# Optimization experiments

Hardware: AMD Instinct MI355X
Metric: run time of the kernel (lower is better)

The kernel has to match this reference:

```python
import jax, jax.numpy as jnp
import numpy as np

N_NODES = 200_000
N_EDGES = 400_000
EXTRA_NNZ = 3 * N_EDGES
IN_CH = 14
HID = 128
ALPHA = -1.5  # HNHN edge-cardinality exponent
BETA = -0.5   # HNHN node-cardinality exponent


def setup_inputs() -> dict:
    key = jax.random.key(0)
    ks = jax.random.split(key, 16)
    # COO incidence: guarantee every node and every edge has >= 1 entry so
    # cardinality^negative_power stays finite (like real molecular hypergraphs).
    base_rows = jnp.arange(N_NODES, dtype=jnp.int32)
    base_cols = jnp.arange(N_NODES, dtype=jnp.int32) % N_EDGES
    edge_rows = jax.random.randint(ks[0], (N_EDGES,), 0, N_NODES, dtype=jnp.int32)
    edge_cols = jnp.arange(N_EDGES, dtype=jnp.int32)
    rnd_rows = jax.random.randint(ks[1], (EXTRA_NNZ,), 0, N_NODES, dtype=jnp.int32)
    rnd_cols = jax.random.randint(ks[2], (EXTRA_NNZ,), 0, N_EDGES, dtype=jnp.int32)
    inc_rows = jnp.concatenate([base_rows, edge_rows, rnd_rows])
    inc_cols = jnp.concatenate([base_cols, edge_cols, rnd_cols])
    inc_vals = jnp.ones(inc_rows.shape[0], dtype=jnp.float32)

    def glorot(k, shape):
        fan_in, fan_out = shape[0], shape[-1]
        s = jnp.sqrt(2.0 / (fan_in + fan_out)).astype(jnp.float32)
        return jax.random.normal(k, shape, dtype=jnp.float32) * s

    return {
        "x_0": jax.random.normal(ks[3], (N_NODES, IN_CH), dtype=jnp.float32),
        "inc_rows": inc_rows,
        "inc_cols": inc_cols,
        "inc_vals": inc_vals,
        "w0_l1": glorot(ks[4], (IN_CH, HID)),
        "w1_l1": glorot(ks[5], (HID, HID)),
        "b1_l1": glorot(ks[6], (1, HID)),
        "b0_l1": glorot(ks[7], (1, HID)),
        "w0_l2": glorot(ks[8], (HID, HID)),
        "w1_l2": glorot(ks[9], (HID, HID)),
        "b1_l2": glorot(ks[10], (1, HID)),
        "b0_l2": glorot(ks[11], (1, HID)),
        "lin_w": glorot(ks[12], (HID, 1)),
        "lin_b": jnp.zeros((1,), dtype=jnp.float32),
    }


def _normalized_values(inc_rows, inc_cols, inc_vals):
    """HNHN alpha/beta normalization of B (node<-edge) and B^T (edge<-node)."""
    seg = jax.ops.segment_sum
    deg_e = seg(inc_vals, inc_cols, num_segments=N_EDGES)   # |e| per hyperedge
    deg_v = seg(inc_vals, inc_rows, num_segments=N_NODES)   # |v| per node
    e_card = deg_e ** ALPHA
    n_card = deg_v ** BETA
    denom_v = seg(inc_vals * e_card[inc_cols], inc_rows, num_segments=N_NODES)  # (B @ e_card)
    denom_e = seg(inc_vals * n_card[inc_rows], inc_cols, num_segments=N_EDGES)  # (B^T @ n_card)
    # D0_left_alpha^{-1} B D1_right_alpha   and   D1_left_beta^{-1} B^T D0_right_beta
    vals_v_from_e = inc_vals * e_card[inc_cols] / denom_v[inc_rows]
    vals_e_from_v = inc_vals * n_card[inc_rows] / denom_e[inc_cols]
    return vals_v_from_e, vals_e_from_v


def reference(x_0, inc_rows, inc_cols, inc_vals,
              w0_l1, w1_l1, b1_l1, b0_l1,
              w0_l2, w1_l2, b1_l2, b0_l2,
              lin_w, lin_b):
    seg = jax.ops.segment_sum
    vals_v_from_e, vals_e_from_v = _normalized_values(inc_rows, inc_cols, inc_vals)

    def layer(x0, w0, w1, b1, b0):
        # node -> hyperedge: x1 = sigma(Bt_norm @ (x0 W0) + b1)
        m = x0 @ w0                                        # [N_NODES, HID]
        x1 = jax.nn.sigmoid(
            seg(vals_e_from_v[:, None] * m[inc_rows], inc_cols, num_segments=N_EDGES) + b1
        )                                                  # [N_EDGES, HID]
        # hyperedge -> node: x0' = sigma(B_norm @ (x1 W1) + b0)
        m2 = x1 @ w1
        x0n = jax.nn.sigmoid(
            seg(vals_v_from_e[:, None] * m2[inc_cols], inc_rows, num_segments=N_NODES) + b0
        )                                                  # [N_NODES, HID]
        return x0n, x1

    x0, x1 = layer(x_0, w0_l1, w1_l1, b1_l1, b0_l1)
    x0, x1 = layer(x0, w0_l2, w1_l2, b1_l2, b0_l2)
    pooled = jnp.max(x0, axis=0)                           # graph-level max pool [HID]
    return pooled @ lin_w + lin_b                          # [1]
```

## Files before the change

### kernel.cpp

```cpp
#include <hip/hip_runtime.h>
#include <hip/hip_bf16.h>

#define N_NODES 200000
#define N_EDGES 400000
#define HID 128

#define SHIFT 10
#define NB_E 391
#define NB_V 196
#define NBT (NB_E + NB_V)
#define CAP_E 6144
#define CAP_V 10240

typedef unsigned int u32;
typedef unsigned short u16;
typedef unsigned char u8;
typedef long long i64;
typedef __attribute__((ext_vector_type(4))) float f32x4;
typedef __attribute__((ext_vector_type(2))) float f32x2;

__device__ inline float sigmoidf(float v) { return 1.0f / (1.0f + __expf(-v)); }

__device__ inline u32 pk4_fp8(float f0, float f1, float f2, float f3) {
  u32 v = __builtin_amdgcn_cvt_pk_fp8_f32(f0, f1, 0, false);
  v = __builtin_amdgcn_cvt_pk_fp8_f32(f2, f3, v, true);
  return v;
}

__device__ inline void acc16_fp8(const uint4& q, float wv, f32x2* a) {
#pragma unroll
  for (int h = 0; h < 4; ++h) {
    u32 u = (&q.x)[h];
    a[h * 2 + 0] += __builtin_amdgcn_cvt_pk_f32_fp8(u, false) * wv;
    a[h * 2 + 1] += __builtin_amdgcn_cvt_pk_f32_fp8(u, true) * wv;
  }
}

__global__ __launch_bounds__(256) void bin_mm14_kernel(
    const int* __restrict__ rows, const int* __restrict__ cols,
    const float* __restrict__ vals, u32* __restrict__ bkE,
    u32* __restrict__ bkV, int2* __restrict__ tmp_e, int2* __restrict__ tmp_v,
    int nnz, int nbBin, const float* __restrict__ x0,
    const float* __restrict__ w14, u8* __restrict__ U, int N) {
  __shared__ u32 smem[14 * HID];
  const int tid = threadIdx.x;

  if ((int)blockIdx.x >= nbBin) {
    float* ws = (float*)smem;
    for (int i = tid; i < 14 * HID; i += 256) ws[i] = w14[i];
    __syncthreads();
    const int row = ((int)blockIdx.x - nbBin) * 8 + (tid >> 5);
    const int c4 = (tid & 31) << 2;
    if (row >= N) return;
    const float* xr = x0 + (size_t)row * 14;
    float a0 = 0.f, a1 = 0.f, a2 = 0.f, a3 = 0.f;
#pragma unroll
    for (int k = 0; k < 14; ++k) {
      const float xv = xr[k];
      const float* wr = ws + k * HID + c4;
      a0 = fmaf(xv, wr[0], a0);
      a1 = fmaf(xv, wr[1], a1);
      a2 = fmaf(xv, wr[2], a2);
      a3 = fmaf(xv, wr[3], a3);
    }
    *(u32*)(U + (size_t)row * HID + c4) = pk4_fp8(a0, a1, a2, a3);
    return;
  }

  u32* h = smem;
  u32* base = smem + NBT;
  for (int j = tid; j < NBT; j += 256) h[j] = 0;
  __syncthreads();
  const int i0 = blockIdx.x * 4096;
  for (int k = 0; k < 16; ++k) {
    int i = i0 + k * 256 + tid;
    if (i < nnz) {
      atomicAdd(&h[cols[i] >> SHIFT], 1u);
      atomicAdd(&h[NB_E + (rows[i] >> SHIFT)], 1u);
    }
  }
  __syncthreads();
  for (int j = tid; j < NBT; j += 256) {
    u32 n = h[j];
    base[j] = n ? ((j < NB_E) ? atomicAdd(&bkE[j], n)
                              : atomicAdd(&bkV[j - NB_E], n))
                : 0;
    h[j] = 0;
  }
  __syncthreads();
  for (int k = 0; k < 16; ++k) {
    int i = i0 + k * 256 + tid;
    if (i < nnz) {
      int c = cols[i], r = rows[i];
      int vb = __float_as_int(vals[i]);
      int be = c >> SHIFT;
      int bv = NB_E + (r >> SHIFT);
      u32 le = atomicAdd(&h[be], 1u);
      tmp_e[(size_t)be * CAP_E + base[be] + le] =
          make_int2(((c & 1023) << 19) | r, vb);
      u32 lv = atomicAdd(&h[bv], 1u);
      tmp_v[(size_t)(bv - NB_E) * CAP_V + base[bv] + lv] =
          make_int2(((r & 1023) << 19) | c, vb);
    }
  }
}

__global__ __launch_bounds__(512) void scan_all_kernel(
    u32* __restrict__ bkE, u32* __restrict__ bkV, u32* __restrict__ ptr_e,
    u32* __restrict__ ptr_v, u32 nnz) {
  if (blockIdx.x == 2) {
    if (threadIdx.x == 0) {
      bkE[NB_E] = nnz;
      bkV[NB_V] = nnz;
      ptr_e[N_EDGES] = nnz;
      ptr_v[N_NODES] = nnz;
    }
    return;
  }
  u32* blk = (blockIdx.x == 0) ? bkE : bkV;
  const int n = (blockIdx.x == 0) ? NB_E : NB_V;
  __shared__ u32 tmp[512];
  int t = threadIdx.x;
  u32 v = (t < n) ? blk[t] : 0;
  tmp[t] = v;
  __syncthreads();
  for (int d = 1; d < 512; d <<= 1) {
    u32 x = (t >= d) ? tmp[t - d] : 0;
    __syncthreads();
    tmp[t] += x;
    __syncthreads();
  }
  if (t < n) blk[t] = tmp[t] - v;
}

template <bool EDGE>
__global__ __launch_bounds__(512) void build_kernel(
    const int2* __restrict__ tmp, int cap, const u32* __restrict__ bukBase,
    u32* __restrict__ ptr, int2* __restrict__ ent, float* __restrict__ card,
    const float* __restrict__ ncard, int S) {
  __shared__ u32 loc[1024];
  __shared__ u32 sstart[1024];
  __shared__ u32 aux[512];
  const int tid = threadIdx.x;
  const int c0 = blockIdx.x << SHIFT;
  const int nseg = min(1024, S - c0);
  const u32 eb = bukBase[blockIdx.x], ee = bukBase[blockIdx.x + 1];
  const u32 cnt = ee - eb;
  const int2* tp = tmp + (size_t)blockIdx.x * cap;
  loc[tid] = 0;
  loc[tid + 512] = 0;
  __syncthreads();
  for (u32 j = tid; j < cnt; j += 512)
    atomicAdd(&loc[(u32)tp[j].x >> 19], 1u);
  __syncthreads();
  u32 a0 = loc[2 * tid], a1 = loc[2 * tid + 1];
  u32 T = a0 + a1;
  aux[tid] = T;
  __syncthreads();
  for (int d = 1; d < 512; d <<= 1) {
    u32 x = (tid >= d) ? aux[tid - d] : 0;
    __syncthreads();
    aux[tid] += x;
    __syncthreads();
  }
  u32 off = aux[tid] - T;
  loc[2 * tid] = off;
  loc[2 * tid + 1] = off + a0;
  sstart[2 * tid] = off;
  sstart[2 * tid + 1] = off + a0;
  __syncthreads();
  for (int k = tid; k < nseg; k += 512) ptr[c0 + k] = eb + loc[k];
  __syncthreads();
  for (u32 j = tid; j < cnt; j += 512) {
    int2 e = tp[j];
    u32 s = (u32)e.x >> 19;
    u32 p = atomicAdd(&loc[s], 1u);
    ent[eb + p] = make_int2(e.x & 0x7FFFF, e.y);
  }
  __syncthreads();
  for (int k = tid; k < nseg; k += 512) {
    u32 s0 = eb + sstart[k], s1 = eb + loc[k];
    float s = 0.f;
    for (u32 j = s0; j < s1; ++j) s += __int_as_float(ent[j].y);
    float t = rsqrtf(s);
    card[c0 + k] = EDGE ? t * t * t : t;
    if (EDGE) {
      float d = 0.f;
      for (u32 j = s0; j < s1; ++j) {
        int2 en = ent[j];
        d += __int_as_float(en.y) * ncard[en.x];
      }
      float inv = 1.f / d;
      for (u32 j = s0; j < s1; ++j) {
        int2 en = ent[j];
        ent[j].y = __float_as_int(__int_as_float(en.y) * ncard[en.x] * inv);
      }
    }
  }
}

__global__ __launch_bounds__(256) void segV_kernel(
    const u32* __restrict__ ptr_v, int2* __restrict__ ent_v,
    const float* __restrict__ e_card) {
  int t = blockIdx.x * 256 + threadIdx.x;
  int i = t >> 1;
  int half = t & 1;
  if (i >= N_NODES) return;
  u32 b = ptr_v[i], e = ptr_v[i + 1];
  float s = 0.f;
  for (u32 j = b + half; j < e; j += 2) {
    int2 en = ent_v[j];
    s += __int_as_float(en.y) * e_card[en.x];
  }
  s += __shfl_xor(s, 1);
  float inv = 1.f / s;
  for (u32 j = b + half; j < e; j += 2) {
    int2 en = ent_v[j];
    ent_v[j].y = __float_as_int(__int_as_float(en.y) * e_card[en.x] * inv);
  }
}


__device__ inline void load_wfrags(const float* __restrict__ w, int lo, int hi,
                                   i64 wf[8][4]) {
#pragma unroll
  for (int n = 0; n < 8; ++n)
#pragma unroll
    for (int t = 0; t < 4; ++t) {
      const float* wp = w + (size_t)(t * 32 + hi * 8) * HID + n * 16 + lo;
      u32 w0 = pk4_fp8(wp[0], wp[HID], wp[2 * HID], wp[3 * HID]);
      u32 w1 = pk4_fp8(wp[4 * HID], wp[5 * HID], wp[6 * HID], wp[7 * HID]);
      wf[n][t] = (i64)w0 | ((i64)w1 << 32);
    }
}

template <bool SIG, bool POOL>
__global__ __launch_bounds__(256, 1) void im128_mfma_kernel(
    u8* __restrict__ buf, const float* __restrict__ w,
    const float* __restrict__ b, u32* __restrict__ pooled, int R) {
  const int tid = threadIdx.x;
  const int wave = tid >> 6;
  const int lo = tid & 15;
  const int hi = (tid & 63) >> 4;
  i64 wf[8][4];
  load_wfrags(w, lo, hi, wf);
  float bias[8];
  if (SIG) {
#pragma unroll
    for (int n = 0; n < 8; ++n) bias[n] = b[n * 16 + lo];
  }
  float pm[8];
#pragma unroll
  for (int n = 0; n < 8; ++n) pm[n] = 0.f;

  for (int rb = blockIdx.x * 64 + wave * 16; rb < R; rb += gridDim.x * 64) {
    const u8* xp = buf + (size_t)(rb + lo) * HID + hi * 8;
    i64 a0 = *(const i64*)(xp);
    i64 a1 = *(const i64*)(xp + 32);
    i64 a2 = *(const i64*)(xp + 64);
    i64 a3 = *(const i64*)(xp + 96);
    u8* yp = buf + (size_t)(rb + hi * 4) * HID + lo;
#pragma unroll
    for (int n = 0; n < 8; ++n) {
      f32x4 c = {0.f, 0.f, 0.f, 0.f};
      c = __builtin_amdgcn_mfma_f32_16x16x32_fp8_fp8(a0, wf[n][0], c, 0, 0, 0);
      c = __builtin_amdgcn_mfma_f32_16x16x32_fp8_fp8(a1, wf[n][1], c, 0, 0, 0);
      c = __builtin_amdgcn_mfma_f32_16x16x32_fp8_fp8(a2, wf[n][2], c, 0, 0, 0);
      c = __builtin_amdgcn_mfma_f32_16x16x32_fp8_fp8(a3, wf[n][3], c, 0, 0, 0);
#pragma unroll
      for (int r = 0; r < 4; ++r) {
        float v = SIG ? sigmoidf(c[r] + bias[n]) : c[r];
        if (POOL) {
          pm[n] = fmaxf(pm[n], v);
        } else {
          u32 q = __builtin_amdgcn_cvt_pk_fp8_f32(v, v, 0, false);
          yp[(size_t)r * HID + n * 16] = (u8)q;
        }
      }
    }
  }

  if (POOL) {
    __shared__ u32 pmax[HID];
    for (int i = tid; i < HID; i += 256) pmax[i] = 0;
    __syncthreads();
#pragma unroll
    for (int n = 0; n < 8; ++n)
      atomicMax(&pmax[n * 16 + lo], __float_as_uint(pm[n]));
    __syncthreads();
    if (tid < HID) atomicMax(&pooled[tid], pmax[tid]);
  }
}


template <bool SIG>
__global__ __launch_bounds__(256) void gather128_kernel(
    const u32* __restrict__ ptr, const int2* __restrict__ ent,
    const u8* __restrict__ src, const float* __restrict__ b,
    u8* __restrict__ dst, int S) {
  long long t = (long long)blockIdx.x * 256 + threadIdx.x;
  int r = (int)(t >> 3);
  if (r >= S) return;
  const int c16 = (int)(t & 7) << 4;
  u32 beg = ptr[r], end = ptr[r + 1];
  f32x2 a[8];
#pragma unroll
  for (int i = 0; i < 8; ++i) a[i] = (f32x2){0.f, 0.f};
  u32 j = beg;
  for (; j + 2 <= end; j += 2) {
    int2 e0 = ent[j];
    int2 e1 = ent[j + 1];
    const uint4 q0 = *(const uint4*)(src + (size_t)e0.x * HID + c16);
    const uint4 q1 = *(const uint4*)(src + (size_t)e1.x * HID + c16);
    acc16_fp8(q0, __int_as_float(e0.y), a);
    acc16_fp8(q1, __int_as_float(e1.y), a);
  }
  if (j < end) {
    int2 e0 = ent[j];
    const uint4 q0 = *(const uint4*)(src + (size_t)e0.x * HID + c16);
    acc16_fp8(q0, __int_as_float(e0.y), a);
  }
  float o[16];
#pragma unroll
  for (int h = 0; h < 4; ++h) {
    o[h * 4 + 0] = a[h * 2 + 0].x;
    o[h * 4 + 1] = a[h * 2 + 0].y;
    o[h * 4 + 2] = a[h * 2 + 1].x;
    o[h * 4 + 3] = a[h * 2 + 1].y;
  }
  if (SIG) {
#pragma unroll
    for (int h = 0; h < 4; ++h) {
      float4 bb = *(const float4*)(b + c16 + h * 4);
      o[h * 4 + 0] = sigmoidf(o[h * 4 + 0] + bb.x);
      o[h * 4 + 1] = sigmoidf(o[h * 4 + 1] + bb.y);
      o[h * 4 + 2] = sigmoidf(o[h * 4 + 2] + bb.z);
      o[h * 4 + 3] = sigmoidf(o[h * 4 + 3] + bb.w);
    }
  }
  uint4 pk;
  pk.x = pk4_fp8(o[0], o[1], o[2], o[3]);
  pk.y = pk4_fp8(o[4], o[5], o[6], o[7]);
  pk.z = pk4_fp8(o[8], o[9], o[10], o[11]);
  pk.w = pk4_fp8(o[12], o[13], o[14], o[15]);
  *(uint4*)(dst + (size_t)r * HID + c16) = pk;
}


__global__ __launch_bounds__(128) void final_kernel(
    const u32* __restrict__ pooled, const float* __restrict__ lin_w,
    const float* __restrict__ lin_b, float* __restrict__ out) {
  __shared__ float red[64];
  int t = threadIdx.x;
  float v = __uint_as_float(pooled[t]) * lin_w[t];
  if (t >= 64) red[t - 64] = v;
  __syncthreads();
  if (t < 64) {
    v += red[t];
#pragma unroll
    for (int off = 32; off > 0; off >>= 1) v += __shfl_down(v, off);
    if (t == 0) out[0] = v + lin_b[0];
  }
}

__global__ void diag_kernel(float* out, float v) { out[0] = v; }


extern "C" void kernel_launch(void* const* d_in, const int* in_sizes, int n_in,
                              void* d_out, int out_size, void* d_ws, size_t ws_size,
                              hipStream_t stream) {
  const float* x0     = (const float*)d_in[0];
  const int*   rows   = (const int*)d_in[1];
  const int*   cols   = (const int*)d_in[2];
  const float* vals   = (const float*)d_in[3];
  const float* w0_l1  = (const float*)d_in[4];
  const float* w1_l1  = (const float*)d_in[5];
  const float* b1_l1  = (const float*)d_in[6];
  const float* b0_l1  = (const float*)d_in[7];
  const float* w0_l2  = (const float*)d_in[8];
  const float* w1_l2  = (const float*)d_in[9];
  const float* b1_l2  = (const float*)d_in[10];
  const float* b0_l2  = (const float*)d_in[11];
  const float* lin_w  = (const float*)d_in[12];
  const float* lin_b  = (const float*)d_in[13];
  float* out = (float*)d_out;
  const int nnz = in_sizes[1];

  char* wsp = (char*)d_ws;
  size_t off = 0;
  auto carve = [&](size_t bytes) -> char* {
    char* p = wsp + off;
    off = (off + bytes + 511) & ~(size_t)511;
    return p;
  };
  float* n_card  = (float*)carve((size_t)N_NODES * 4);
  float* e_card  = (float*)carve((size_t)N_EDGES * 4);
  u32*   ptr_v   = (u32*)carve((size_t)(N_NODES + 1) * 4);
  u32*   ptr_e   = (u32*)carve((size_t)(N_EDGES + 1) * 4);
  u32*   bkE     = (u32*)carve((NB_E + 1) * 4);
  u32*   bkV     = (u32*)carve((NB_V + 1) * 4);
  int2*  ent_v   = (int2*)carve((size_t)nnz * 8);
  int2*  ent_e   = (int2*)carve((size_t)nnz * 8);
  u32*   pooled  = (u32*)carve(HID * 4);
  u8*    bufN    = (u8*)carve((size_t)N_NODES * HID);
  u8*    bufE    = (u8*)carve((size_t)N_EDGES * HID);
  int2*  tmp_e   = (int2*)carve((size_t)NB_E * CAP_E * 8);
  int2*  tmp_v   = (int2*)carve((size_t)NB_V * CAP_V * 8);

  if (off > ws_size) {
    diag_kernel<<<1, 1, 0, stream>>>(out, (float)(ws_size >> 20));
    return;
  }

  hipMemsetAsync(bkE, 0, (NB_E + 1) * 4, stream);
  hipMemsetAsync(bkV, 0, (NB_V + 1) * 4, stream);
  hipMemsetAsync(pooled, 0, HID * 4, stream);

  const int nbBin = (nnz + 4095) / 4096;
  const int nbMM14 = (N_NODES + 7) / 8;

  bin_mm14_kernel<<<nbBin + nbMM14, 256, 0, stream>>>(
      rows, cols, vals, bkE, bkV, tmp_e, tmp_v, nnz, nbBin,
      x0, w0_l1, bufN, N_NODES);
  scan_all_kernel<<<3, 512, 0, stream>>>(bkE, bkV, ptr_e, ptr_v, (u32)nnz);
  build_kernel<false><<<NB_V, 512, 0, stream>>>(tmp_v, CAP_V, bkV, ptr_v,
                                                ent_v, n_card, nullptr, N_NODES);
  build_kernel<true><<<NB_E, 512, 0, stream>>>(tmp_e, CAP_E, bkE, ptr_e,
                                               ent_e, e_card, n_card, N_EDGES);
  segV_kernel<<<(2 * N_NODES + 255) / 256, 256, 0, stream>>>(ptr_v, ent_v, e_card);

  const int nbE8 = (int)(((long long)N_EDGES * 8 + 255) / 256);
  const int nbN8 = (int)(((long long)N_NODES * 8 + 255) / 256);

  gather128_kernel<true><<<nbE8, 256, 0, stream>>>(ptr_e, ent_e, bufN,
                                                   b1_l1, bufE, N_EDGES);
  gather128_kernel<false><<<nbN8, 256, 0, stream>>>(ptr_v, ent_v, bufE,
                                                    nullptr, bufN, N_NODES);
  im128_mfma_kernel<true, false><<<1024, 256, 0, stream>>>(bufN, w1_l1, b0_l1,
                                                           nullptr, N_NODES);

  im128_mfma_kernel<false, false><<<1024, 256, 0, stream>>>(bufN, w0_l2, nullptr,
                                                            nullptr, N_NODES);
  gather128_kernel<true><<<nbE8, 256, 0, stream>>>(ptr_e, ent_e, bufN,
                                                   b1_l2, bufE, N_EDGES);
  gather128_kernel<false><<<nbN8, 256, 0, stream>>>(ptr_v, ent_v, bufE,
                                                    nullptr, bufN, N_NODES);
  im128_mfma_kernel<true, true><<<1024, 256, 0, stream>>>(bufN, w1_l2, b0_l2,
                                                          pooled, N_NODES);

  final_kernel<<<1, 128, 0, stream>>>(pooled, lin_w, lin_b, out);
}
```

Measured before the change: 453.4 us.

## Split binning into per-direction blocks with LDS-staged coalesced scatter

Measured after the change: 498.2 us. 9.9% more time.

```diff
diff --git a/kernel.cpp b/kernel.cpp
--- a/kernel.cpp
+++ b/kernel.cpp
@@ -8,9 +8,9 @@
 #define SHIFT 10
 #define NB_E 391
 #define NB_V 196
-#define NBT (NB_E + NB_V)
 #define CAP_E 6144
 #define CAP_V 10240
+#define BINSZ 4096
 
 typedef unsigned int u32;
 typedef unsigned short u16;
@@ -40,16 +40,22 @@
     const int* __restrict__ rows, const int* __restrict__ cols,
     const float* __restrict__ vals, u32* __restrict__ bkE,
     u32* __restrict__ bkV, int2* __restrict__ tmp_e, int2* __restrict__ tmp_v,
-    int nnz, int nbBin, const float* __restrict__ x0,
+    int nnz, int nbBinE, int nbBinV, const float* __restrict__ x0,
     const float* __restrict__ w14, u8* __restrict__ U, int N) {
-  __shared__ u32 smem[14 * HID];
+  __shared__ int2 stage[BINSZ];
+  __shared__ u32 dsti[BINSZ];
+  __shared__ u32 h[NB_E];
+  __shared__ u32 pe[NB_E + 1];
+  __shared__ u32 gb[NB_E];
+  __shared__ u32 aux[256];
   const int tid = threadIdx.x;
-
-  if ((int)blockIdx.x >= nbBin) {
-    float* ws = (float*)smem;
+  const int bid = blockIdx.x;
+
+  if (bid >= nbBinE + nbBinV) {
+    float* ws = (float*)stage;
     for (int i = tid; i < 14 * HID; i += 256) ws[i] = w14[i];
     __syncthreads();
-    const int row = ((int)blockIdx.x - nbBin) * 8 + (tid >> 5);
+    const int row = (bid - nbBinE - nbBinV) * 8 + (tid >> 5);
     const int c4 = (tid & 31) << 2;
     if (row >= N) return;
     const float* xr = x0 + (size_t)row * 14;
@@ -67,48 +73,67 @@
     return;
   }
 
-  u32* h = smem;
-  u32* base = smem + NBT;
-  for (int j = tid; j < NBT; j += 256) h[j] = 0;
-  __syncthreads();
-  const int i0 = blockIdx.x * 4096;
-  for (int k = 0; k < 16; ++k) {
+  const bool ES = bid < nbBinE;
+  const int blk = ES ? bid : bid - nbBinE;
+  const int NB = ES ? NB_E : NB_V;
+  const int CAP = ES ? CAP_E : CAP_V;
+  const int* __restrict__ key = ES ? cols : rows;
+  const int* __restrict__ oth = ES ? rows : cols;
+  u32* __restrict__ bk = ES ? bkE : bkV;
+  int2* __restrict__ tmp = ES ? tmp_e : tmp_v;
+
+  for (int j = tid; j < NB; j += 256) h[j] = 0;
+  __syncthreads();
+  const int i0 = blk * BINSZ;
+  const int total = min(BINSZ, nnz - i0);
+#pragma unroll
+  for (int k = 0; k < BINSZ / 256; ++k) {
+    int i = i0 + k * 256 + tid;
+    if (i < nnz) atomicAdd(&h[key[i] >> SHIFT], 1u);
+  }
+  __syncthreads();
+  u32 a0 = (2 * tid < NB) ? h[2 * tid] : 0;
+  u32 a1 = (2 * tid + 1 < NB) ? h[2 * tid + 1] : 0;
+  u32 T = a0 + a1;
+  aux[tid] = T;
+  __syncthreads();
+  for (int d = 1; d < 256; d <<= 1) {
+    u32 x = (tid >= d) ? aux[tid - d] : 0;
+    __syncthreads();
+    aux[tid] += x;
+    __syncthreads();
+  }
+  u32 off = aux[tid] - T;
+  if (2 * tid < NB) pe[2 * tid] = off;
+  if (2 * tid + 1 < NB) pe[2 * tid + 1] = off + a0;
+  for (int j = tid; j < NB; j += 256) {
+    u32 n = h[j];
+    gb[j] = n ? atomicAdd(&bk[j], n) : 0;
+    h[j] = 0;
+  }
+  __syncthreads();
+#pragma unroll
+  for (int k = 0; k < BINSZ / 256; ++k) {
     int i = i0 + k * 256 + tid;
     if (i < nnz) {
-      atomicAdd(&h[cols[i] >> SHIFT], 1u);
-      atomicAdd(&h[NB_E + (rows[i] >> SHIFT)], 1u);
-    }
-  }
-  __syncthreads();
-  for (int j = tid; j < NBT; j += 256) {
-    u32 n = h[j];
-    base[j] = n ? ((j < NB_E) ? atomicAdd(&bkE[j], n)
-                              : atomicAdd(&bkV[j - NB_E], n))
-                : 0;
-    h[j] = 0;
-  }
-  __syncthreads();
-  for (int k = 0; k < 16; ++k) {
-    int i = i0 + k * 256 + tid;
-    if (i < nnz) {
-      int c = cols[i], r = rows[i];
-      int vb = __float_as_int(vals[i]);
-      int be = c >> SHIFT;
-      int bv = NB_E + (r >> SHIFT);
-      u32 le = atomicAdd(&h[be], 1u);
-      tmp_e[(size_t)be * CAP_E + base[be] + le] =
-          make_int2(((c & 1023) << 19) | r, vb);
-      u32 lv = atomicAdd(&h[bv], 1u);
-      tmp_v[(size_t)(bv - NB_E) * CAP_V + base[bv] + lv] =
-          make_int2(((r & 1023) << 19) | c, vb);
-    }
-  }
+      int kk = key[i];
+      int b = kk >> SHIFT;
+      u32 lr = atomicAdd(&h[b], 1u);
+      u32 pos = pe[b] + lr;
+      stage[pos] = make_int2(((kk & 1023) << 19) | oth[i],
+                             __float_as_int(vals[i]));
+      dsti[pos] = (u32)b * CAP + gb[b] + lr;
+    }
+  }
+  __syncthreads();
+  for (int t = tid; t < total; t += 256) tmp[dsti[t]] = stage[t];
 }
 
 __global__ __launch_bounds__(512) void scan_all_kernel(
     u32* __restrict__ bkE, u32* __restrict__ bkV, u32* __restrict__ ptr_e,
-    u32* __restrict__ ptr_v, u32 nnz) {
+    u32* __restrict__ ptr_v, u32* __restrict__ pooled, u32 nnz) {
   if (blockIdx.x == 2) {
+    if (threadIdx.x < HID) pooled[threadIdx.x] = 0;
     if (threadIdx.x == 0) {
       bkE[NB_E] = nnz;
       bkV[NB_V] = nnz;
@@ -412,17 +437,15 @@
     return;
   }
 
-  hipMemsetAsync(bkE, 0, (NB_E + 1) * 4, stream);
-  hipMemsetAsync(bkV, 0, (NB_V + 1) * 4, stream);
-  hipMemsetAsync(pooled, 0, HID * 4, stream);
-
-  const int nbBin = (nnz + 4095) / 4096;
+  hipMemsetAsync(bkE, 0, (size_t)((char*)ent_v - (char*)bkE), stream);
+
+  const int nbBin = (nnz + BINSZ - 1) / BINSZ;
   const int nbMM14 = (N_NODES + 7) / 8;
 
-  bin_mm14_kernel<<<nbBin + nbMM14, 256, 0, stream>>>(
-      rows, cols, vals, bkE, bkV, tmp_e, tmp_v, nnz, nbBin,
+  bin_mm14_kernel<<<2 * nbBin + nbMM14, 256, 0, stream>>>(
+      rows, cols, vals, bkE, bkV, tmp_e, tmp_v, nnz, nbBin, nbBin,
       x0, w0_l1, bufN, N_NODES);
-  scan_all_kernel<<<3, 512, 0, stream>>>(bkE, bkV, ptr_e, ptr_v, (u32)nnz);
+  scan_all_kernel<<<3, 512, 0, stream>>>(bkE, bkV, ptr_e, ptr_v, pooled, (u32)nnz);
   build_kernel<false><<<NB_V, 512, 0, stream>>>(tmp_v, CAP_V, bkV, ptr_v,
                                                 ent_v, n_card, nullptr, N_NODES);
   build_kernel<true><<<NB_E, 512, 0, stream>>>(tmp_e, CAP_E, bkE, ptr_e,
```

## Reorder gather rows by segment length to balance wavefront work

Applied to the files above, without the earlier changes.

New measurement: 478.3 us. 1.05x slower.

```diff
diff --git a/kernel.cpp b/kernel.cpp
--- a/kernel.cpp
+++ b/kernel.cpp
@@ -11,6 +11,7 @@
 #define NBT (NB_E + NB_V)
 #define CAP_E 6144
 #define CAP_V 10240
+#define BINSZ 4096
 
 typedef unsigned int u32;
 typedef unsigned short u16;
@@ -71,8 +72,8 @@
   u32* base = smem + NBT;
   for (int j = tid; j < NBT; j += 256) h[j] = 0;
   __syncthreads();
-  const int i0 = blockIdx.x * 4096;
-  for (int k = 0; k < 16; ++k) {
+  const int i0 = blockIdx.x * BINSZ;
+  for (int k = 0; k < BINSZ / 256; ++k) {
     int i = i0 + k * 256 + tid;
     if (i < nnz) {
       atomicAdd(&h[cols[i] >> SHIFT], 1u);
@@ -88,7 +89,7 @@
     h[j] = 0;
   }
   __syncthreads();
-  for (int k = 0; k < 16; ++k) {
+  for (int k = 0; k < BINSZ / 256; ++k) {
     int i = i0 + k * 256 + tid;
     if (i < nnz) {
       int c = cols[i], r = rows[i];
@@ -107,8 +108,9 @@
 
 __global__ __launch_bounds__(512) void scan_all_kernel(
     u32* __restrict__ bkE, u32* __restrict__ bkV, u32* __restrict__ ptr_e,
-    u32* __restrict__ ptr_v, u32 nnz) {
+    u32* __restrict__ ptr_v, u32* __restrict__ pooled, u32 nnz) {
   if (blockIdx.x == 2) {
+    if (threadIdx.x < HID) pooled[threadIdx.x] = 0;
     if (threadIdx.x == 0) {
       bkE[NB_E] = nnz;
       bkV[NB_V] = nnz;
@@ -137,10 +139,11 @@
 __global__ __launch_bounds__(512) void build_kernel(
     const int2* __restrict__ tmp, int cap, const u32* __restrict__ bukBase,
     u32* __restrict__ ptr, int2* __restrict__ ent, float* __restrict__ card,
-    const float* __restrict__ ncard, int S) {
+    const float* __restrict__ ncard, u32* __restrict__ lcnt, int S) {
   __shared__ u32 loc[1024];
   __shared__ u32 sstart[1024];
   __shared__ u32 aux[512];
+  __shared__ u32 lh[16];
   const int tid = threadIdx.x;
   const int c0 = blockIdx.x << SHIFT;
   const int nseg = min(1024, S - c0);
@@ -149,6 +152,7 @@
   const int2* tp = tmp + (size_t)blockIdx.x * cap;
   loc[tid] = 0;
   loc[tid + 512] = 0;
+  if (tid < 16) lh[tid] = 0;
   __syncthreads();
   for (u32 j = tid; j < cnt; j += 512)
     atomicAdd(&loc[(u32)tp[j].x >> 19], 1u);
@@ -179,6 +183,8 @@
   }
   __syncthreads();
   for (int k = tid; k < nseg; k += 512) {
+    u32 len = loc[k] - sstart[k];
+    atomicAdd(&lh[min(len - 1, 15u)], 1u);
     u32 s0 = eb + sstart[k], s1 = eb + loc[k];
     float s = 0.f;
     for (u32 j = s0; j < s1; ++j) s += __int_as_float(ent[j].y);
@@ -197,6 +203,48 @@
       }
     }
   }
+  __syncthreads();
+  if (tid < 16 && lh[tid]) atomicAdd(&lcnt[tid], lh[tid]);
+}
+
+__global__ void scan32_kernel(u32* __restrict__ lcntE, u32* __restrict__ lcntV) {
+  u32* a = (threadIdx.x == 0) ? lcntE : lcntV;
+  u32 s = 0;
+  for (int i = 0; i < 16; ++i) {
+    u32 v = a[i];
+    a[i] = s;
+    s += v;
+  }
+}
+
+__global__ __launch_bounds__(256) void perm_place_kernel(
+    const u32* __restrict__ ptr_e, const u32* __restrict__ ptr_v,
+    u32* __restrict__ curE, u32* __restrict__ curV,
+    u32* __restrict__ permE, u32* __restrict__ permV, int nbE) {
+  const int bid = blockIdx.x;
+  const bool ES = bid < nbE;
+  const u32* ptr = ES ? ptr_e : ptr_v;
+  u32* cur = ES ? curE : curV;
+  u32* perm = ES ? permE : permV;
+  const int S = ES ? N_EDGES : N_NODES;
+  const int i = (ES ? bid : bid - nbE) * 256 + threadIdx.x;
+  __shared__ u32 lh[16];
+  __shared__ u32 base[16];
+  if (threadIdx.x < 16) lh[threadIdx.x] = 0;
+  __syncthreads();
+  int b = 0;
+  u32 lr = 0;
+  if (i < S) {
+    u32 len = ptr[i + 1] - ptr[i];
+    b = (int)min(len - 1, 15u);
+    lr = atomicAdd(&lh[b], 1u);
+  }
+  __syncthreads();
+  if (threadIdx.x < 16)
+    base[threadIdx.x] =
+        lh[threadIdx.x] ? atomicAdd(&cur[threadIdx.x], lh[threadIdx.x]) : 0;
+  __syncthreads();
+  if (i < S) perm[base[b] + lr] = (u32)i;
 }
 
 __global__ __launch_bounds__(256) void segV_kernel(
@@ -296,11 +344,12 @@
 template <bool SIG>
 __global__ __launch_bounds__(256) void gather128_kernel(
     const u32* __restrict__ ptr, const int2* __restrict__ ent,
-    const u8* __restrict__ src, const float* __restrict__ b,
-    u8* __restrict__ dst, int S) {
+    const u32* __restrict__ perm, const u8* __restrict__ src,
+    const float* __restrict__ b, u8* __restrict__ dst, int S) {
   long long t = (long long)blockIdx.x * 256 + threadIdx.x;
-  int r = (int)(t >> 3);
-  if (r >= S) return;
+  int rid = (int)(t >> 3);
+  if (rid >= S) return;
+  const int r = (int)perm[rid];
   const int c16 = (int)(t & 7) << 4;
   u32 beg = ptr[r], end = ptr[r + 1];
   f32x2 a[8];
@@ -399,8 +448,12 @@
   u32*   ptr_e   = (u32*)carve((size_t)(N_EDGES + 1) * 4);
   u32*   bkE     = (u32*)carve((NB_E + 1) * 4);
   u32*   bkV     = (u32*)carve((NB_V + 1) * 4);
+  u32*   lcntE   = (u32*)carve(16 * 4);
+  u32*   lcntV   = (u32*)carve(16 * 4);
   int2*  ent_v   = (int2*)carve((size_t)nnz * 8);
   int2*  ent_e   = (int2*)carve((size_t)nnz * 8);
+  u32*   permE   = (u32*)carve((size_t)N_EDGES * 4);
+  u32*   permV   = (u32*)carve((size_t)N_NODES * 4);
   u32*   pooled  = (u32*)carve(HID * 4);
   u8*    bufN    = (u8*)carve((size_t)N_NODES * HID);
   u8*    bufE    = (u8*)carve((size_t)N_EDGES * HID);
@@ -412,38 +465,41 @@
     return;
   }
 
-  hipMemsetAsync(bkE, 0, (NB_E + 1) * 4, stream);
-  hipMemsetAsync(bkV, 0, (NB_V + 1) * 4, stream);
-  hipMemsetAsync(pooled, 0, HID * 4, stream);
-
-  const int nbBin = (nnz + 4095) / 4096;
+  hipMemsetAsync(bkE, 0, (size_t)((char*)ent_v - (char*)bkE), stream);
+
+  const int nbBin = (nnz + BINSZ - 1) / BINSZ;
   const int nbMM14 = (N_NODES + 7) / 8;
+  const int nbPermE = (N_EDGES + 255) / 256;
+  const int nbPermV = (N_NODES + 255) / 256;
 
   bin_mm14_kernel<<<nbBin + nbMM14, 256, 0, stream>>>(
       rows, cols, vals, bkE, bkV, tmp_e, tmp_v, nnz, nbBin,
       x0, w0_l1, bufN, N_NODES);
-  scan_all_kernel<<<3, 512, 0, stream>>>(bkE, bkV, ptr_e, ptr_v, (u32)nnz);
-  build_kernel<false><<<NB_V, 512, 0, stream>>>(tmp_v, CAP_V, bkV, ptr_v,
-                                                ent_v, n_card, nullptr, N_NODES);
-  build_kernel<true><<<NB_E, 512, 0, stream>>>(tmp_e, CAP_E, bkE, ptr_e,
-                                               ent_e, e_card, n_card, N_EDGES);
+  scan_all_kernel<<<3, 512, 0, stream>>>(bkE, bkV, ptr_e, ptr_v, pooled, (u32)nnz);
+  build_kernel<false><<<NB_V, 512, 0, stream>>>(tmp_v, CAP_V, bkV, ptr_v, ent_v,
+                                                n_card, nullptr, lcntV, N_NODES);
+  build_kernel<true><<<NB_E, 512, 0, stream>>>(tmp_e, CAP_E, bkE, ptr_e, ent_e,
+                                               e_card, n_card, lcntE, N_EDGES);
+  scan32_kernel<<<1, 2, 0, stream>>>(lcntE, lcntV);
+  perm_place_kernel<<<nbPermE + nbPermV, 256, 0, stream>>>(
+      ptr_e, ptr_v, lcntE, lcntV, permE, permV, nbPermE);
   segV_kernel<<<(2 * N_NODES + 255) / 256, 256, 0, stream>>>(ptr_v, ent_v, e_card);
 
   const int nbE8 = (int)(((long long)N_EDGES * 8 + 255) / 256);
   const int nbN8 = (int)(((long long)N_NODES * 8 + 255) / 256);
 
-  gather128_kernel<true><<<nbE8, 256, 0, stream>>>(ptr_e, ent_e, bufN,
+  gather128_kernel<true><<<nbE8, 256, 0, stream>>>(ptr_e, ent_e, permE, bufN,
                                                    b1_l1, bufE, N_EDGES);
-  gather128_kernel<false><<<nbN8, 256, 0, stream>>>(ptr_v, ent_v, bufE,
+  gather128_kernel<false><<<nbN8, 256, 0, stream>>>(ptr_v, ent_v, permV, bufE,
                                                     nullptr, bufN, N_NODES);
   im128_mfma_kernel<true, false><<<1024, 256, 0, stream>>>(bufN, w1_l1, b0_l1,
                                                            nullptr, N_NODES);
 
   im128_mfma_kernel<false, false><<<1024, 256, 0, stream>>>(bufN, w0_l2, nullptr,
                                                             nullptr, N_NODES);
-  gather128_kernel<true><<<nbE8, 256, 0, stream>>>(ptr_e, ent_e, bufN,
+  gather128_kernel<true><<<nbE8, 256, 0, stream>>>(ptr_e, ent_e, permE, bufN,
                                                    b1_l2, bufE, N_EDGES);
-  gather128_kernel<false><<<nbN8, 256, 0, stream>>>(ptr_v, ent_v, bufE,
+  gather128_kernel<false><<<nbN8, 256, 0, stream>>>(ptr_v, ent_v, permV, bufE,
                                                     nullptr, bufN, N_NODES);
   im128_mfma_kernel<true, true><<<1024, 256, 0, stream>>>(bufN, w1_l2, b0_l2,
                                                           pooled, N_NODES);
```
